# Optimization experiments

Hardware: AMD Instinct MI355X
Metric: run time of the kernel (lower is better)

The kernel has to match this reference:

```python
import jax, jax.numpy as jnp
import numpy as np

V, E, D, FN, FE, G = 20000, 100000, 32, 36, 12, 1000
DEPTH, S2S_ITERS = 3, 6


def setup_inputs() -> dict:
    key = jax.random.key(0)
    ks = jax.random.split(key, 30)
    rn = lambda k, s, sc=0.1: (jax.random.normal(k, s, jnp.float32) * sc)
    inp = {
        "node": jax.random.normal(ks[0], (V, FN), jnp.float32),
        "edge": jax.random.normal(ks[1], (E, FE), jnp.float32),
        "src": jax.random.randint(ks[2], (V,) if False else (E,), 0, V, jnp.int32),
        "dst": jax.random.randint(ks[3], (E,), 0, V, jnp.int32),
        "node2graph": jnp.sort(jax.random.randint(ks[4], (V,), 0, G, jnp.int32)),
        # embeddings
        "Wn": rn(ks[5], (FN, D)), "bn": jnp.zeros((D,), jnp.float32),
        "We": rn(ks[6], (FE, D)), "be": jnp.zeros((D,), jnp.float32),
        # per-layer edge network (stacked over depth)
        "eW1": rn(ks[7], (DEPTH, D, 2 * D)), "eb1": jnp.zeros((DEPTH, 2 * D), jnp.float32),
        "eW2": rn(ks[8], (DEPTH, 2 * D, D * D), 0.02), "eb2": jnp.zeros((DEPTH, D * D), jnp.float32),
        # per-layer GRUCell (torch layout: [3D, in])
        "gru_wih": rn(ks[9], (DEPTH, 3 * D, D)), "gru_whh": rn(ks[10], (DEPTH, 3 * D, D)),
        "gru_bih": jnp.zeros((DEPTH, 3 * D), jnp.float32), "gru_bhh": jnp.zeros((DEPTH, 3 * D), jnp.float32),
        # per-layer LayerNorm
        "ln_g": jnp.ones((DEPTH, D), jnp.float32), "ln_b": jnp.zeros((DEPTH, D), jnp.float32),
        # Set2Set LSTMCell: input 2D -> hidden D (torch gate order i,f,g,o)
        "lstm_wih": rn(ks[11], (4 * D, 2 * D)), "lstm_whh": rn(ks[12], (4 * D, D)),
        "lstm_bih": jnp.zeros((4 * D,), jnp.float32), "lstm_bhh": jnp.zeros((4 * D,), jnp.float32),
        # prediction MLP
        "Wp1": rn(ks[13], (2 * D, D)), "bp1": jnp.zeros((D,), jnp.float32),
        "Wp2": rn(ks[14], (D, 1)), "bp2": jnp.zeros((1,), jnp.float32),
    }
    return inp


def _leaky(x):
    return jnp.where(x > 0, x, 0.01 * x)


def _forward(node, edge, src, dst, node2graph, Wn, bn, We, be, eW1, eb1, eW2, eb2,
             gru_wih, gru_whh, gru_bih, gru_bhh, ln_g, ln_b,
             lstm_wih, lstm_whh, lstm_bih, lstm_bhh, Wp1, bp1, Wp2, bp2):
    h = _leaky(node @ Wn + bn)            # (V, D) embedded nodes
    e_h = _leaky(edge @ We + be)          # (E, D) embedded edges
    hidden0 = h                           # GRU hidden is the initial embedding (never updated in source)
    for l in range(DEPTH):
        # edge-conditioned weights: (E, D, D)
        ew = jax.nn.relu(e_h @ eW1[l] + eb1[l]) @ eW2[l] + eb2[l]
        Wmat = ew.reshape(E, D, D)
        msg = jnp.einsum('ed,edf->ef', h[src], Wmat)          # gather + per-edge matmul
        agg = jax.ops.segment_sum(msg, dst, num_segments=V)   # scatter-sum to dst nodes
        agg = jax.nn.relu(agg)
        # torch GRUCell(agg, hidden0)
        gi = agg @ gru_wih[l].T + gru_bih[l]
        gh = hidden0 @ gru_whh[l].T + gru_bhh[l]
        ir, iz, inn = jnp.split(gi, 3, axis=-1)
        hr, hz, hn = jnp.split(gh, 3, axis=-1)
        r = jax.nn.sigmoid(ir + hr)
        z = jax.nn.sigmoid(iz + hz)
        n = jnp.tanh(inn + r * hn)
        hnew = (1.0 - z) * n + z * hidden0
        # LayerNorm
        mu = hnew.mean(-1, keepdims=True)
        var = ((hnew - mu) ** 2).mean(-1, keepdims=True)
        h = (hnew - mu) * jax.lax.rsqrt(var + 1e-5) * ln_g[l] + ln_b[l]
    # Set2Set readout over graphs
    q_star = jnp.zeros((G, 2 * D), jnp.float32)
    hh = jnp.zeros((G, D), jnp.float32)
    cc = jnp.zeros((G, D), jnp.float32)
    for _ in range(S2S_ITERS):
        gates = q_star @ lstm_wih.T + lstm_bih + hh @ lstm_whh.T + lstm_bhh
        i, f, g, o = jnp.split(gates, 4, axis=-1)
        cc = jax.nn.sigmoid(f) * cc + jax.nn.sigmoid(i) * jnp.tanh(g)
        hh = jax.nn.sigmoid(o) * jnp.tanh(cc)
        q = hh                                                 # (G, D)
        att = jnp.sum(h * q[node2graph], axis=-1)              # (V,)
        m = jax.ops.segment_max(att, node2graph, num_segments=G)
        ex = jnp.exp(att - m[node2graph])
        denom = jax.ops.segment_sum(ex, node2graph, num_segments=G)
        alpha = ex / denom[node2graph]
        r_read = jax.ops.segment_sum(alpha[:, None] * h, node2graph, num_segments=G)
        q_star = jnp.concatenate([q, r_read], axis=-1)
    out = jax.nn.relu(q_star @ Wp1 + bp1) @ Wp2 + bp2          # (G, 1)
    return out


def reference(node, edge, src, dst, node2graph, Wn, bn, We, be, eW1, eb1, eW2, eb2,
              gru_wih, gru_whh, gru_bih, gru_bhh, ln_g, ln_b,
              lstm_wih, lstm_whh, lstm_bih, lstm_bhh, Wp1, bp1, Wp2, bp2):
    return _forward(node, edge, src, dst, node2graph, Wn, bn, We, be, eW1, eb1, eW2, eb2,
                    gru_wih, gru_whh, gru_bih, gru_bhh, ln_g, ln_b,
                    lstm_wih, lstm_whh, lstm_bih, lstm_bhh, Wp1, bp1, Wp2, bp2)
```

## Files before the change

kernel.cpp:

```cpp
#include <hip/hip_runtime.h>
#include <math.h>

#define NV 20000
#define NE 100000
#define DD 32
#define NG 1000
#define NDEPTH 3
#define S2S 6
#define NBK 8
#define EPB 16
#define CAPN 128
#define SCAN_T 256
#define SCAN_C 80

__device__ __forceinline__ float sigmoidf_(float x) { return 1.0f / (1.0f + __expf(-x)); }

__global__ void k_prolog(const float* __restrict__ node, const float* __restrict__ Wn,
                         const float* __restrict__ bn, float* __restrict__ h,
                         float* __restrict__ h0,
                         const float* __restrict__ edge, const float* __restrict__ We,
                         const float* __restrict__ be, float* __restrict__ e_h,
                         const int* __restrict__ n2g, int* __restrict__ gstart,
                         int* __restrict__ deg) {
    __shared__ float sWn[36 * DD];
    __shared__ float sbn[DD];
    __shared__ float sxn[32][36];
    __shared__ float sWe[12 * DD];
    __shared__ float sbe[DD];
    __shared__ float sxe[32][12];
    int tid = threadIdx.x;
    int b = blockIdx.x;
    if (b < 625) {
        for (int i = tid; i < 36 * DD; i += 256) sWn[i] = Wn[i];
        if (tid < DD) sbn[tid] = bn[tid];
        int v0 = b * 32;
        for (int i = tid; i < 32 * 36; i += 256) sxn[i / 36][i % 36] = node[(size_t)v0 * 36 + i];
        __syncthreads();
        int f = tid & 31;
        int nb = tid >> 5;
        for (int g = 0; g < 4; ++g) {
            int n = nb + 8 * g;
            float acc = sbn[f];
            #pragma unroll
            for (int i = 0; i < 36; ++i) acc += sxn[n][i] * sWn[i * DD + f];
            float y = acc > 0.f ? acc : 0.01f * acc;
            h[(size_t)(v0 + n) * DD + f] = y;
            h0[(size_t)(v0 + n) * DD + f] = y;
        }
    } else if (b < 3750) {
        for (int i = tid; i < 12 * DD; i += 256) sWe[i] = We[i];
        if (tid < DD) sbe[tid] = be[tid];
        int e0 = (b - 625) * 32;
        for (int i = tid; i < 32 * 12; i += 256) sxe[i / 12][i % 12] = edge[(size_t)e0 * 12 + i];
        __syncthreads();
        int f = tid & 31;
        int nb = tid >> 5;
        for (int g = 0; g < 4; ++g) {
            int n = nb + 8 * g;
            float acc = sbe[f];
            #pragma unroll
            for (int i = 0; i < 12; ++i) acc += sxe[n][i] * sWe[i * DD + f];
            float y = acc > 0.f ? acc : 0.01f * acc;
            e_h[(size_t)(e0 + n) * DD + f] = y;
        }
    } else if (b < 3755) {
        int g = (b - 3750) * 256 + tid;
        if (g <= NG) {
            int lo = 0, hi = NV;
            while (lo < hi) {
                int mid = (lo + hi) >> 1;
                if (n2g[mid] < g) lo = mid + 1; else hi = mid;
            }
            gstart[g] = lo;
        }
    } else {
        int i = (b - 3755) * 256 + tid;
        if (i < NV) deg[i] = 0;
    }
}

__global__ void k_hist(const int* __restrict__ src, int* __restrict__ deg) {
    int e = blockIdx.x * blockDim.x + threadIdx.x;
    if (e < NE) atomicAdd(&deg[src[e]], 1);
}

__global__ void k_scan(const int* __restrict__ deg, int* __restrict__ estart, int* __restrict__ cur) {
    __shared__ int sdeg[SCAN_T * SCAN_C];
    __shared__ int spart[SCAN_T];
    int tid = threadIdx.x;
    for (int i = tid; i < SCAN_T * SCAN_C; i += SCAN_T) sdeg[i] = (i < NV) ? deg[i] : 0;
    __syncthreads();
    int base = tid * SCAN_C;
    int sum = 0;
    for (int j = 0; j < SCAN_C; ++j) sum += sdeg[base + j];
    spart[tid] = sum;
    __syncthreads();
    for (int off = 1; off < SCAN_T; off <<= 1) {
        int v = (tid >= off) ? spart[tid - off] : 0;
        __syncthreads();
        spart[tid] += v;
        __syncthreads();
    }
    int run = spart[tid] - sum;
    for (int j = 0; j < SCAN_C; ++j) {
        int idx = base + j;
        if (idx < NV) { estart[idx] = run; cur[idx] = run; }
        run += sdeg[base + j];
    }
    if (tid == SCAN_T - 1) estart[NV] = run;
}

__global__ void k_scatter(const int* __restrict__ src, int* __restrict__ cur,
                          int* __restrict__ esorted) {
    int e = blockIdx.x * blockDim.x + threadIdx.x;
    if (e < NE) {
        int s = src[e];
        int pos = atomicAdd(&cur[s], 1);
        esorted[pos] = e;
    }
}

__global__ void k_edge_t3(const float* __restrict__ e_h, const float* __restrict__ eW1,
                          const float* __restrict__ eb1, float* __restrict__ t3,
                          float* __restrict__ agg) {
    __shared__ float sW[DD * 64];
    __shared__ float sb[64];
    int tid = threadIdx.x;
    int b = blockIdx.x;
    if (b < (NV * DD) / 256) agg[(size_t)b * 256 + tid] = 0.f;
    int l = b / 6250, bb = b % 6250;
    const float* W = eW1 + (size_t)l * DD * 64;
    float* t = t3 + (size_t)l * NE * 64;
    for (int i = tid; i < DD * 64; i += 256) sW[i] = W[i];
    if (tid < 64) sb[tid] = eb1[l * 64 + tid];
    int e0 = bb * EPB;
    __syncthreads();
    int k = tid & 63;
    int nb = tid >> 6;
    float acc[4];
    #pragma unroll
    for (int g = 0; g < 4; ++g) acc[g] = sb[k];
    #pragma unroll
    for (int d4 = 0; d4 < 8; ++d4) {
        float4 ex[4];
        #pragma unroll
        for (int g = 0; g < 4; ++g)
            ex[g] = *(const float4*)(e_h + (size_t)(e0 + nb + 4 * g) * DD + d4 * 4);
        #pragma unroll
        for (int dd = 0; dd < 4; ++dd) {
            float w = sW[(d4 * 4 + dd) * 64 + k];
            #pragma unroll
            for (int g = 0; g < 4; ++g)
                acc[g] = fmaf((&ex[g].x)[dd], w, acc[g]);
        }
    }
    #pragma unroll
    for (int g = 0; g < 4; ++g)
        t[(size_t)(e0 + nb + 4 * g) * 64 + k] = fmaxf(acc[g], 0.f);
}

__global__ __launch_bounds__(1024, 8) void k_fused(const float* __restrict__ h,
        const float* __restrict__ eW2, const float* __restrict__ eb2,
        const float* __restrict__ t, const int* __restrict__ dst,
        const int* __restrict__ estart, const int* __restrict__ esorted,
        float* __restrict__ agg) {
    int v0 = blockIdx.x * NBK;
    __shared__ float sA[NBK][64][32];
    __shared__ float sbb[NBK][32];
    int tid = threadIdx.x;
    int lane = tid & 63;

    float4 hv4 = *(const float4*)(h + (size_t)(v0 + (lane >> 3)) * DD + 4 * (lane & 7));
    float ha[4] = {hv4.x, hv4.y, hv4.z, hv4.w};

    int f = tid & 31;
    int kb = tid >> 5;
    const float* wbase = eW2 + kb * 1024 + f;

    float acc[2][8];
    #pragma unroll
    for (int jj = 0; jj < 2; ++jj)
        #pragma unroll
        for (int n = 0; n < 8; ++n) acc[jj][n] = 0.f;

    #pragma unroll
    for (int d4 = 0; d4 < 8; ++d4) {
        float hs[8][4];
        #pragma unroll
        for (int n = 0; n < 8; ++n)
            #pragma unroll
            for (int dd = 0; dd < 4; ++dd)
                hs[n][dd] = __builtin_bit_cast(float,
                    __builtin_amdgcn_readlane(__builtin_bit_cast(int, ha[dd]), n * 8 + d4));
        #pragma unroll
        for (int jj = 0; jj < 2; ++jj) {
            const float* wp = wbase + jj * 32 * 1024 + d4 * 4 * 32;
            #pragma unroll
            for (int dd = 0; dd < 4; ++dd) {
                float w = wp[dd * 32];
                #pragma unroll
                for (int n = 0; n < 8; ++n) acc[jj][n] = fmaf(hs[n][dd], w, acc[jj][n]);
            }
        }
    }
    #pragma unroll
    for (int jj = 0; jj < 2; ++jj)
        #pragma unroll
        for (int n = 0; n < 8; ++n)
            sA[n][kb + 32 * jj][f] = acc[jj][n];

    if (tid < 256) {
        int n = tid >> 5;
        float bacc = 0.f;
        #pragma unroll
        for (int d = 0; d < DD; ++d) {
            float hvv = __shfl(ha[d & 3], n * 8 + (d >> 2), 64);
            bacc = fmaf(hvv, eb2[d * 32 + f], bacc);
        }
        sbb[n][f] = bacc;
    }
    __syncthreads();

    int w = tid >> 6;
    int n = w >> 1;
    int par = w & 1;
    int hf = lane >> 5;
    float Areg[32];
    #pragma unroll
    for (int q = 0; q < 32; ++q)
        Areg[q] = sA[n][2 * q + hf][f];
    float bbv = sbb[n][f];
    int i = estart[v0 + n] + par, e1 = estart[v0 + n + 1];
    if (i < e1) {
        int e = esorted[i];
        float tv = t[(size_t)e * 64 + lane];
        int dn = dst[e];
        while (i < e1) {
            i += 2;
            float tv2 = 0.f; int dn2 = 0;
            if (i < e1) {
                int e2 = esorted[i];
                tv2 = t[(size_t)e2 * 64 + lane];
                dn2 = dst[e2];
            }
            float m0 = 0.f, m1 = 0.f, m2 = 0.f, m3 = 0.f;
            #pragma unroll
            for (int q = 0; q < 32; q += 4) {
                m0 = fmaf(__shfl(tv, 2 * q + hf, 64),       Areg[q],     m0);
                m1 = fmaf(__shfl(tv, 2 * (q + 1) + hf, 64), Areg[q + 1], m1);
                m2 = fmaf(__shfl(tv, 2 * (q + 2) + hf, 64), Areg[q + 2], m2);
                m3 = fmaf(__shfl(tv, 2 * (q + 3) + hf, 64), Areg[q + 3], m3);
            }
            float m = (m0 + m1) + (m2 + m3);
            m += __shfl_xor(m, 32, 64);
            if (lane < 32) atomicAdd(&agg[(size_t)dn * DD + f], m + bbv);
            tv = tv2; dn = dn2;
        }
    }
}

__global__ __launch_bounds__(256, 2) void k_gru_ln(float* __restrict__ agg,
                         const float* __restrict__ h0,
                         const float* __restrict__ wih, const float* __restrict__ whh,
                         const float* __restrict__ bih, const float* __restrict__ bhh,
                         const float* __restrict__ lng, const float* __restrict__ lnb,
                         float* __restrict__ h) {
    __shared__ float sWT[2][3][32][33];
    __shared__ float sbih[96], sbhh[96], sg[DD], sb[DD];
    int tid = threadIdx.x;
    for (int i = tid; i < 3072; i += 256) {
        int g = i >> 10, j = (i >> 5) & 31, f = i & 31;
        sWT[0][g][f][j] = wih[i];
        sWT[1][g][f][j] = whh[i];
    }
    if (tid < 96) { sbih[tid] = bih[tid]; sbhh[tid] = bhh[tid]; }
    if (tid < DD) { sg[tid] = lng[tid]; sb[tid] = lnb[tid]; }
    int v0 = blockIdx.x * 8;
    __syncthreads();
    int j = tid & 31;
    int n = v0 + (tid >> 5);
    float4 aq[8], hq[8];
    #pragma unroll
    for (int f4 = 0; f4 < 8; ++f4) {
        float4 a = *(const float4*)(agg + (size_t)n * DD + f4 * 4);
        a.x = fmaxf(a.x, 0.f); a.y = fmaxf(a.y, 0.f); a.z = fmaxf(a.z, 0.f); a.w = fmaxf(a.w, 0.f);
        aq[f4] = a;
        hq[f4] = *(const float4*)(h0 + (size_t)n * DD + f4 * 4);
    }
    agg[(size_t)n * DD + j] = 0.f;
    float h0j = h0[(size_t)n * DD + j];
    float gi0 = 0.f, gi1 = 0.f, gi2 = 0.f, gh0 = 0.f, gh1 = 0.f, gh2 = 0.f;
    #pragma unroll
    for (int f4 = 0; f4 < 8; ++f4) {
        #pragma unroll
        for (int dd = 0; dd < 4; ++dd) {
            int f = f4 * 4 + dd;
            float a = (&aq[f4].x)[dd], hh = (&hq[f4].x)[dd];
            gi0 = fmaf(a, sWT[0][0][f][j], gi0);
            gi1 = fmaf(a, sWT[0][1][f][j], gi1);
            gi2 = fmaf(a, sWT[0][2][f][j], gi2);
            gh0 = fmaf(hh, sWT[1][0][f][j], gh0);
            gh1 = fmaf(hh, sWT[1][1][f][j], gh1);
            gh2 = fmaf(hh, sWT[1][2][f][j], gh2);
        }
    }
    float r = sigmoidf_(gi0 + sbih[j] + gh0 + sbhh[j]);
    float z = sigmoidf_(gi1 + sbih[DD + j] + gh1 + sbhh[DD + j]);
    float nn = tanhf(gi2 + sbih[2 * DD + j] + r * (gh2 + sbhh[2 * DD + j]));
    float hnew = (1.f - z) * nn + z * h0j;
    float mu = hnew;
    #pragma unroll
    for (int o = 16; o; o >>= 1) mu += __shfl_xor(mu, o, 64);
    mu *= (1.f / DD);
    float d = hnew - mu;
    float var = d * d;
    #pragma unroll
    for (int o = 16; o; o >>= 1) var += __shfl_xor(var, o, 64);
    var *= (1.f / DD);
    float inv = rsqrtf(var + 1e-5f);
    h[(size_t)n * DD + j] = d * inv * sg[j] + sb[j];
}

__global__ __launch_bounds__(256) void k_s2s(const float* __restrict__ h,
                      const int* __restrict__ gstart,
                      const float* __restrict__ wih, const float* __restrict__ whh,
                      const float* __restrict__ bih, const float* __restrict__ bhh,
                      const float* __restrict__ Wp1, const float* __restrict__ bp1,
                      const float* __restrict__ Wp2, const float* __restrict__ bp2,
                      float* __restrict__ attbuf, float* __restrict__ out) {
    int g = blockIdx.x, tid = threadIdx.x;
    int s = gstart[g], e = gstart[g + 1], cnt = e - s;
    bool inlds = (cnt <= CAPN);
    __shared__ float sh[CAPN * 33];
    __shared__ float qs[64], shh[32], scc[32], gbuf[128];
    __shared__ float satt[256];
    __shared__ float red[4];
    __shared__ float rpart[8][32];
    if (inlds) {
        for (int idx = tid; idx < cnt * 32; idx += 256) {
            int v = idx >> 5, f = idx & 31;
            sh[v * 33 + f] = h[(size_t)(s + v) * 32 + f];
        }
    }
    if (tid < 64) qs[tid] = 0.f;
    if (tid < 32) { shh[tid] = 0.f; scc[tid] = 0.f; }
    __syncthreads();
    for (int it = 0; it < S2S; ++it) {
        if (tid < 128) {
            float gv = bih[tid] + bhh[tid];
            const float4* w4 = (const float4*)(wih + tid * 64);
            #pragma unroll
            for (int i = 0; i < 16; ++i) {
                float4 w = w4[i];
                gv += qs[4 * i] * w.x + qs[4 * i + 1] * w.y + qs[4 * i + 2] * w.z + qs[4 * i + 3] * w.w;
            }
            const float4* u4 = (const float4*)(whh + tid * 32);
            #pragma unroll
            for (int i = 0; i < 8; ++i) {
                float4 w = u4[i];
                gv += shh[4 * i] * w.x + shh[4 * i + 1] * w.y + shh[4 * i + 2] * w.z + shh[4 * i + 3] * w.w;
            }
            gbuf[tid] = gv;
        }
        __syncthreads();
        if (tid < 32) {
            float ii = gbuf[tid], ff = gbuf[32 + tid], gg = gbuf[64 + tid], oo = gbuf[96 + tid];
            float c = sigmoidf_(ff) * scc[tid] + sigmoidf_(ii) * tanhf(gg);
            scc[tid] = c;
            float hv = sigmoidf_(oo) * tanhf(c);
            shh[tid] = hv;
            qs[tid] = hv;
        }
        __syncthreads();
        float pmax = -1e30f;
        if (inlds) {
            float a = -1e30f;
            if (tid < cnt) {
                float acc = 0.f;
                #pragma unroll
                for (int f = 0; f < 32; ++f) acc += sh[tid * 33 + f] * shh[f];
                a = acc;
            }
            satt[tid] = a;
            pmax = a;
        } else {
            for (int v = tid; v < cnt; v += 256) {
                float acc = 0.f;
                const float* hp = h + (size_t)(s + v) * 32;
                #pragma unroll
                for (int f = 0; f < 32; ++f) acc += hp[f] * shh[f];
                attbuf[s + v] = acc;
                pmax = fmaxf(pmax, acc);
            }
        }
        #pragma unroll
        for (int o = 32; o; o >>= 1) pmax = fmaxf(pmax, __shfl_xor(pmax, o, 64));
        if ((tid & 63) == 0) red[tid >> 6] = pmax;
        __syncthreads();
        float m = fmaxf(fmaxf(red[0], red[1]), fmaxf(red[2], red[3]));
        float psum = 0.f;
        if (inlds) {
            if (tid < cnt) { float exv = __expf(satt[tid] - m); satt[tid] = exv; psum = exv; }
        } else {
            for (int v = tid; v < cnt; v += 256) {
                float exv = __expf(attbuf[s + v] - m); attbuf[s + v] = exv; psum += exv;
            }
        }
        #pragma unroll
        for (int o = 32; o; o >>= 1) psum += __shfl_xor(psum, o, 64);
        __syncthreads();
        if ((tid & 63) == 0) red[tid >> 6] = psum;
        __syncthreads();
        float denom = red[0] + red[1] + red[2] + red[3];
        int f = tid & 31, vc = tid >> 5;
        float racc = 0.f;
        if (inlds) {
            for (int v = vc; v < cnt; v += 8) racc += satt[v] * sh[v * 33 + f];
        } else {
            for (int v = vc; v < cnt; v += 8) racc += attbuf[s + v] * h[(size_t)(s + v) * 32 + f];
        }
        rpart[vc][f] = racc;
        __syncthreads();
        if (tid < 32) {
            float r = 0.f;
            #pragma unroll
            for (int c2 = 0; c2 < 8; ++c2) r += rpart[c2][tid];
            qs[32 + tid] = (cnt > 0) ? (r / denom) : 0.f;
        }
        __syncthreads();
    }
    if (tid < 32) {
        float u = bp1[tid];
        #pragma unroll
        for (int p = 0; p < 64; ++p) u += qs[p] * Wp1[p * 32 + tid];
        u = fmaxf(u, 0.f);
        float pr = u * Wp2[tid];
        #pragma unroll
        for (int o = 16; o; o >>= 1) pr += __shfl_xor(pr, o, 64);
        if (tid == 0) out[g] = pr + bp2[0];
    }
}

extern "C" void kernel_launch(void* const* d_in, const int* in_sizes, int n_in,
                              void* d_out, int out_size, void* d_ws, size_t ws_size,
                              hipStream_t stream) {
    const float* node = (const float*)d_in[0];
    const float* edge = (const float*)d_in[1];
    const int*   src  = (const int*)d_in[2];
    const int*   dst  = (const int*)d_in[3];
    const int*   n2g  = (const int*)d_in[4];
    const float* Wn   = (const float*)d_in[5];
    const float* bn   = (const float*)d_in[6];
    const float* We   = (const float*)d_in[7];
    const float* be   = (const float*)d_in[8];
    const float* eW1  = (const float*)d_in[9];
    const float* eb1  = (const float*)d_in[10];
    const float* eW2  = (const float*)d_in[11];
    const float* eb2  = (const float*)d_in[12];
    const float* gwih = (const float*)d_in[13];
    const float* gwhh = (const float*)d_in[14];
    const float* gbih = (const float*)d_in[15];
    const float* gbhh = (const float*)d_in[16];
    const float* lng  = (const float*)d_in[17];
    const float* lnb  = (const float*)d_in[18];
    const float* lwih = (const float*)d_in[19];
    const float* lwhh = (const float*)d_in[20];
    const float* lbih = (const float*)d_in[21];
    const float* lbhh = (const float*)d_in[22];
    const float* Wp1  = (const float*)d_in[23];
    const float* bp1  = (const float*)d_in[24];
    const float* Wp2  = (const float*)d_in[25];
    const float* bp2  = (const float*)d_in[26];

    float* ws = (float*)d_ws;
    float* h    = ws; ws += (size_t)NV * DD;
    float* h0   = ws; ws += (size_t)NV * DD;
    float* e_h  = ws; ws += (size_t)NE * DD;
    float* t3   = ws; ws += (size_t)NE * 64 * NDEPTH;
    float* agg  = ws; ws += (size_t)NV * DD;
    float* attbuf = ws; ws += NV;
    int* deg     = (int*)ws; ws += NV;
    int* cur     = (int*)ws; ws += NV;
    int* estart  = (int*)ws; ws += (NV + 1);
    int* esorted = (int*)ws; ws += NE;
    int* gstart  = (int*)ws; ws += (NG + 1);

    k_prolog<<<3755 + (NV + 255) / 256, 256, 0, stream>>>(node, Wn, bn, h, h0,
                                                          edge, We, be, e_h,
                                                          n2g, gstart, deg);
    k_hist<<<(NE + 255) / 256, 256, 0, stream>>>(src, deg);
    k_scan<<<1, SCAN_T, 0, stream>>>(deg, estart, cur);
    k_scatter<<<(NE + 255) / 256, 256, 0, stream>>>(src, cur, esorted);

    k_edge_t3<<<NDEPTH * (NE / EPB), 256, 0, stream>>>(e_h, eW1, eb1, t3, agg);

    for (int l = 0; l < NDEPTH; ++l) {
        k_fused<<<NV / NBK, 1024, 0, stream>>>(h, eW2 + (size_t)l * 64 * 1024, eb2 + l * 1024,
                                               t3 + (size_t)l * NE * 64, dst, estart, esorted, agg);
        k_gru_ln<<<NV / 8, 256, 0, stream>>>(agg, h0,
                                             gwih + (size_t)l * 96 * DD, gwhh + (size_t)l * 96 * DD,
                                             gbih + l * 96, gbhh + l * 96,
                                             lng + l * DD, lnb + l * DD, h);
    }

    k_s2s<<<NG, 256, 0, stream>>>(h, gstart, lwih, lwhh, lbih, lbhh, Wp1, bp1, Wp2, bp2,
                                  attbuf, (float*)d_out);
}
```

Baseline: 573.3 us.

## Fuse GRU+LayerNorm into next layer's message kernel with ping-pong agg buffers

The GRU update and LayerNorm of the previous layer now run at the start of the next layer's fused message kernel, so the updated node state stays in shared memory and is never written to or reread from global h. Two aggregation buffers alternate between layers so one can be read and cleared while the other accumulates. Two separate k_gru_ln launches and their global h round trips go away. The cost is that only 256 of 1024 threads do the GRU work while the rest wait at a barrier, and the GRU weights are read straight from global memory. The edge-embedding kernel also handles 32 edges per block instead of 16.

```diff
diff --git a/kernel.cpp b/kernel.cpp
--- a/kernel.cpp
+++ b/kernel.cpp
@@ -8,7 +8,7 @@
 #define NDEPTH 3
 #define S2S 6
 #define NBK 8
-#define EPB 16
+#define EPB 32
 #define CAPN 128
 #define SCAN_T 256
 #define SCAN_C 80
@@ -122,13 +122,13 @@
 
 __global__ void k_edge_t3(const float* __restrict__ e_h, const float* __restrict__ eW1,
                           const float* __restrict__ eb1, float* __restrict__ t3,
-                          float* __restrict__ agg) {
+                          float* __restrict__ aggAB) {
     __shared__ float sW[DD * 64];
     __shared__ float sb[64];
     int tid = threadIdx.x;
     int b = blockIdx.x;
-    if (b < (NV * DD) / 256) agg[(size_t)b * 256 + tid] = 0.f;
-    int l = b / 6250, bb = b % 6250;
+    if (b < (2 * NV * DD) / 256) aggAB[(size_t)b * 256 + tid] = 0.f;
+    int l = b / (NE / EPB), bb = b % (NE / EPB);
     const float* W = eW1 + (size_t)l * DD * 64;
     float* t = t3 + (size_t)l * NE * 64;
     for (int i = tid; i < DD * 64; i += 256) sW[i] = W[i];
@@ -137,29 +137,34 @@
     __syncthreads();
     int k = tid & 63;
     int nb = tid >> 6;
-    float acc[4];
-    #pragma unroll
-    for (int g = 0; g < 4; ++g) acc[g] = sb[k];
+    float acc[8];
+    #pragma unroll
+    for (int g = 0; g < 8; ++g) acc[g] = sb[k];
     #pragma unroll
     for (int d4 = 0; d4 < 8; ++d4) {
-        float4 ex[4];
-        #pragma unroll
-        for (int g = 0; g < 4; ++g)
+        float4 ex[8];
+        #pragma unroll
+        for (int g = 0; g < 8; ++g)
             ex[g] = *(const float4*)(e_h + (size_t)(e0 + nb + 4 * g) * DD + d4 * 4);
         #pragma unroll
         for (int dd = 0; dd < 4; ++dd) {
             float w = sW[(d4 * 4 + dd) * 64 + k];
             #pragma unroll
-            for (int g = 0; g < 4; ++g)
+            for (int g = 0; g < 8; ++g)
                 acc[g] = fmaf((&ex[g].x)[dd], w, acc[g]);
         }
     }
     #pragma unroll
-    for (int g = 0; g < 4; ++g)
+    for (int g = 0; g < 8; ++g)
         t[(size_t)(e0 + nb + 4 * g) * 64 + k] = fmaxf(acc[g], 0.f);
 }
 
-__global__ __launch_bounds__(1024, 8) void k_fused(const float* __restrict__ h,
+template<int LAYER0>
+__global__ __launch_bounds__(1024, 8) void k_fused_t(const float* __restrict__ hglob,
+        const float* __restrict__ h0, float* __restrict__ aggprev,
+        const float* __restrict__ wih, const float* __restrict__ whh,
+        const float* __restrict__ bih, const float* __restrict__ bhh,
+        const float* __restrict__ lng, const float* __restrict__ lnb,
         const float* __restrict__ eW2, const float* __restrict__ eb2,
         const float* __restrict__ t, const int* __restrict__ dst,
         const int* __restrict__ estart, const int* __restrict__ esorted,
@@ -167,10 +172,62 @@
     int v0 = blockIdx.x * NBK;
     __shared__ float sA[NBK][64][32];
     __shared__ float sbb[NBK][32];
+    __shared__ __align__(16) float hbuf[NBK][32];
     int tid = threadIdx.x;
     int lane = tid & 63;
 
-    float4 hv4 = *(const float4*)(h + (size_t)(v0 + (lane >> 3)) * DD + 4 * (lane & 7));
+    if constexpr (!LAYER0) {
+        if (tid < 256) {
+            int n = tid >> 5, j = tid & 31;
+            int v = v0 + n;
+            float gi0 = 0.f, gi1 = 0.f, gi2 = 0.f, gh0 = 0.f, gh1 = 0.f, gh2 = 0.f;
+            #pragma unroll
+            for (int f4 = 0; f4 < 8; ++f4) {
+                float4 a4 = *(const float4*)(aggprev + (size_t)v * DD + f4 * 4);
+                a4.x = fmaxf(a4.x, 0.f); a4.y = fmaxf(a4.y, 0.f);
+                a4.z = fmaxf(a4.z, 0.f); a4.w = fmaxf(a4.w, 0.f);
+                float4 h4 = *(const float4*)(h0 + (size_t)v * DD + f4 * 4);
+                const float* wb = wih + j * 32 + f4 * 4;
+                float4 wr = *(const float4*)(wb);
+                float4 wz = *(const float4*)(wb + 1024);
+                float4 wn = *(const float4*)(wb + 2048);
+                const float* ub = whh + j * 32 + f4 * 4;
+                float4 ur = *(const float4*)(ub);
+                float4 uz = *(const float4*)(ub + 1024);
+                float4 un = *(const float4*)(ub + 2048);
+                gi0 += a4.x * wr.x + a4.y * wr.y + a4.z * wr.z + a4.w * wr.w;
+                gi1 += a4.x * wz.x + a4.y * wz.y + a4.z * wz.z + a4.w * wz.w;
+                gi2 += a4.x * wn.x + a4.y * wn.y + a4.z * wn.z + a4.w * wn.w;
+                gh0 += h4.x * ur.x + h4.y * ur.y + h4.z * ur.z + h4.w * ur.w;
+                gh1 += h4.x * uz.x + h4.y * uz.y + h4.z * uz.z + h4.w * uz.w;
+                gh2 += h4.x * un.x + h4.y * un.y + h4.z * un.z + h4.w * un.w;
+            }
+            aggprev[(size_t)v * DD + j] = 0.f;
+            float h0j = h0[(size_t)v * DD + j];
+            float r = sigmoidf_(gi0 + bih[j] + gh0 + bhh[j]);
+            float z = sigmoidf_(gi1 + bih[DD + j] + gh1 + bhh[DD + j]);
+            float nn = tanhf(gi2 + bih[2 * DD + j] + r * (gh2 + bhh[2 * DD + j]));
+            float hnew = (1.f - z) * nn + z * h0j;
+            float mu = hnew;
+            #pragma unroll
+            for (int o = 16; o; o >>= 1) mu += __shfl_xor(mu, o, 64);
+            mu *= (1.f / DD);
+            float d = hnew - mu;
+            float var = d * d;
+            #pragma unroll
+            for (int o = 16; o; o >>= 1) var += __shfl_xor(var, o, 64);
+            var *= (1.f / DD);
+            float inv = rsqrtf(var + 1e-5f);
+            hbuf[n][j] = d * inv * lng[j] + lnb[j];
+        }
+        __syncthreads();
+    }
+
+    float4 hv4;
+    if constexpr (LAYER0)
+        hv4 = *(const float4*)(hglob + (size_t)(v0 + (lane >> 3)) * DD + 4 * (lane & 7));
+    else
+        hv4 = *(const float4*)(&hbuf[lane >> 3][4 * (lane & 7)]);
     float ha[4] = {hv4.x, hv4.y, hv4.z, hv4.w};
 
     int f = tid & 31;
@@ -287,7 +344,6 @@
         aq[f4] = a;
         hq[f4] = *(const float4*)(h0 + (size_t)n * DD + f4 * 4);
     }
-    agg[(size_t)n * DD + j] = 0.f;
     float h0j = h0[(size_t)n * DD + j];
     float gi0 = 0.f, gi1 = 0.f, gi2 = 0.f, gh0 = 0.f, gh1 = 0.f, gh2 = 0.f;
     #pragma unroll
@@ -477,7 +533,8 @@
     float* h0   = ws; ws += (size_t)NV * DD;
     float* e_h  = ws; ws += (size_t)NE * DD;
     float* t3   = ws; ws += (size_t)NE * 64 * NDEPTH;
-    float* agg  = ws; ws += (size_t)NV * DD;
+    float* aggA = ws; ws += (size_t)NV * DD;
+    float* aggB = ws; ws += (size_t)NV * DD;
     float* attbuf = ws; ws += NV;
     int* deg     = (int*)ws; ws += NV;
     int* cur     = (int*)ws; ws += NV;
@@ -492,16 +549,23 @@
     k_scan<<<1, SCAN_T, 0, stream>>>(deg, estart, cur);
     k_scatter<<<(NE + 255) / 256, 256, 0, stream>>>(src, cur, esorted);
 
-    k_edge_t3<<<NDEPTH * (NE / EPB), 256, 0, stream>>>(e_h, eW1, eb1, t3, agg);
-
-    for (int l = 0; l < NDEPTH; ++l) {
-        k_fused<<<NV / NBK, 1024, 0, stream>>>(h, eW2 + (size_t)l * 64 * 1024, eb2 + l * 1024,
-                                               t3 + (size_t)l * NE * 64, dst, estart, esorted, agg);
-        k_gru_ln<<<NV / 8, 256, 0, stream>>>(agg, h0,
-                                             gwih + (size_t)l * 96 * DD, gwhh + (size_t)l * 96 * DD,
-                                             gbih + l * 96, gbhh + l * 96,
-                                             lng + l * DD, lnb + l * DD, h);
-    }
+    k_edge_t3<<<NDEPTH * (NE / EPB), 256, 0, stream>>>(e_h, eW1, eb1, t3, aggA);
+
+    k_fused_t<1><<<NV / NBK, 1024, 0, stream>>>(h, h0, nullptr,
+                                                nullptr, nullptr, nullptr, nullptr, nullptr, nullptr,
+                                                eW2, eb2, t3, dst, estart, esorted, aggA);
+    k_fused_t<0><<<NV / NBK, 1024, 0, stream>>>(nullptr, h0, aggA,
+                                                gwih, gwhh, gbih, gbhh, lng, lnb,
+                                                eW2 + 65536, eb2 + 1024,
+                                                t3 + (size_t)NE * 64, dst, estart, esorted, aggB);
+    k_fused_t<0><<<NV / NBK, 1024, 0, stream>>>(nullptr, h0, aggB,
+                                                gwih + 3072, gwhh + 3072, gbih + 96, gbhh + 96,
+                                                lng + DD, lnb + DD,
+                                                eW2 + 131072, eb2 + 2048,
+                                                t3 + (size_t)2 * NE * 64, dst, estart, esorted, aggA);
+    k_gru_ln<<<NV / 8, 256, 0, stream>>>(aggA, h0,
+                                         gwih + 6144, gwhh + 6144, gbih + 192, gbhh + 192,
+                                         lng + 2 * DD, lnb + 2 * DD, h);
 
     k_s2s<<<NG, 256, 0, stream>>>(h, gstart, lwih, lwhh, lbih, lbhh, Wp1, bp1, Wp2, bp2,
                                   attbuf, (float*)d_out);
```

Measured after the change: 860.4 us. 1.5x slower.
